# Kernel optimization log

Measured on AMD Instinct MI355X. Metric: run time of the kernel, lower is better.

The kernel has to match this reference:

```python
import jax, jax.numpy as jnp
import numpy as np
from jax import lax

N, CIN, COUT, KH, KW = 8, 32, 32, 3, 3
AUX, HID = 128, 256

def _prelu(z, a):
    return jnp.where(z >= 0, z, a * z)

def setup_inputs() -> dict:
    key = jax.random.key(0)
    ks = jax.random.split(key, 16)
    k = float(np.sqrt(1.0 / (CIN * KH * KW)))
    x = jax.random.normal(ks[0], (N, CIN, 384, 384), dtype=jnp.float32)
    y = jax.random.normal(ks[1], (N, AUX), dtype=jnp.float32)
    weight = jax.random.uniform(ks[2], (COUT, CIN, KH, KW), minval=-k, maxval=k, dtype=jnp.float32)
    mod_out = COUT * CIN * KH * KW
    s1 = float(np.sqrt(1.0 / AUX)); s2 = float(np.sqrt(1.0 / HID))
    fc_w1 = jax.random.uniform(ks[3], (AUX, HID), minval=-s1, maxval=s1, dtype=jnp.float32)
    fc_b1 = jax.random.uniform(ks[4], (HID,), minval=-s1, maxval=s1, dtype=jnp.float32)
    fc_a = jnp.asarray(0.25, dtype=jnp.float32)  # PReLU default init
    fc_w2 = jax.random.uniform(ks[5], (HID, mod_out), minval=-s2, maxval=s2, dtype=jnp.float32)
    fc_b2 = jax.random.uniform(ks[6], (mod_out,), minval=-s2, maxval=s2, dtype=jnp.float32)
    b_w1 = jax.random.uniform(ks[7], (AUX, HID), minval=-s1, maxval=s1, dtype=jnp.float32)
    b_b1 = jax.random.uniform(ks[8], (HID,), minval=-s1, maxval=s1, dtype=jnp.float32)
    b_a = jnp.asarray(0.25, dtype=jnp.float32)
    b_w2 = jax.random.uniform(ks[9], (HID, COUT), minval=-s2, maxval=s2, dtype=jnp.float32)
    b_b2 = jax.random.uniform(ks[10], (COUT,), minval=-s2, maxval=s2, dtype=jnp.float32)
    return {"x": x, "y": y, "weight": weight,
            "fc_w1": fc_w1, "fc_b1": fc_b1, "fc_a": fc_a, "fc_w2": fc_w2, "fc_b2": fc_b2,
            "b_w1": b_w1, "b_b1": b_b1, "b_a": b_a, "b_w2": b_w2, "b_b2": b_b2}

def reference(x, y, weight, fc_w1, fc_b1, fc_a, fc_w2, fc_b2, b_w1, b_b1, b_a, b_w2, b_b2):
    # Modulation MLP: Linear -> PReLU -> Linear -> Sigmoid
    h = _prelu(y @ fc_w1 + fc_b1, fc_a)
    mod = jax.nn.sigmoid(h @ fc_w2 + fc_b2)            # (N, COUT*CIN*KH*KW)
    w_mod = mod.reshape(N, COUT, CIN, KH, KW) * weight  # per-sample kernels

    # Per-sample conv2d, stride 1, padding 1 (SAME-like for k=3)
    def conv1(xi, wi):  # xi: (CIN,H,W), wi: (COUT,CIN,KH,KW)
        o = lax.conv_general_dilated(xi[None], wi, window_strides=(1, 1),
                                     padding=[(1, 1), (1, 1)],
                                     dimension_numbers=("NCHW", "OIHW", "NCHW"))
        return o[0]
    out = jax.vmap(conv1)(x, w_mod)                     # (N, COUT, H, W)

    # Learned bias MLP: Linear -> PReLU -> Linear
    hb = _prelu(y @ b_w1 + b_b1, b_a)
    bias = hb @ b_w2 + b_b2                             # (N, COUT)
    return out + bias[:, :, None, None]
```

## Files before the change

### kernel.cpp

```cpp
#include <hip/hip_runtime.h>
#include <math.h>

#define N_    8
#define CIN   32
#define COUT  32
#define AUX   128
#define HID   256
#define HWD   384
#define HW2   (HWD*HWD)
#define MODOUT (COUT*CIN*9)

typedef short s8v  __attribute__((ext_vector_type(8)));
typedef float f16v __attribute__((ext_vector_type(16)));

__device__ __forceinline__ unsigned short f2b(float f) {
    unsigned u = __float_as_uint(f);
    u += 0x7FFF + ((u >> 16) & 1);
    return (unsigned short)(u >> 16);
}
__device__ __forceinline__ float prelu_f(float z, float a) { return z >= 0.f ? z : a * z; }

__global__ __launch_bounds__(256) void mlp_head(
    const float* __restrict__ y,
    const float* __restrict__ fc_w1, const float* __restrict__ fc_b1, const float* __restrict__ fc_a,
    const float* __restrict__ b_w1,  const float* __restrict__ b_b1,  const float* __restrict__ b_a,
    const float* __restrict__ b_w2,  const float* __restrict__ b_b2,
    float* __restrict__ ws_h, float* __restrict__ ws_bias)
{
    __shared__ float ly[AUX];
    __shared__ float lhb[HID];
    const int n = blockIdx.x;
    const int j = threadIdx.x;
    if (j < AUX) ly[j] = y[n*AUX + j];
    __syncthreads();
    float ha = fc_b1[j];
    float hb = b_b1[j];
    for (int k = 0; k < AUX; ++k) {
        const float yv = ly[k];
        ha += yv * fc_w1[k*HID + j];
        hb += yv * b_w1[k*HID + j];
    }
    ws_h[n*HID + j] = prelu_f(ha, fc_a[0]);
    lhb[j] = prelu_f(hb, b_a[0]);
    __syncthreads();
    if (j < COUT) {
        float acc = b_b2[j];
        for (int k = 0; k < HID; ++k) acc += lhb[k] * b_w2[k*COUT + j];
        ws_bias[n*COUT + j] = acc;
    }
}

__global__ __launch_bounds__(256) void mod_weights(
    const float* __restrict__ ws_h,
    const float* __restrict__ fc_w2, const float* __restrict__ fc_b2,
    const float* __restrict__ weight, unsigned short* __restrict__ wmod)
{
    __shared__ float lh[N_*HID];
    __shared__ float red[8][32][N_];
    const int tid = threadIdx.x;
    for (int i = tid; i < N_*HID; i += 256) lh[i] = ws_h[i];
    __syncthreads();
    const int ml = tid & 31;
    const int jc = tid >> 5;
    const int m  = blockIdx.x * 32 + ml;
    float acc[N_];
#pragma unroll
    for (int n = 0; n < N_; ++n) acc[n] = 0.f;
    for (int jj = 0; jj < 32; ++jj) {
        const int j = jc*32 + jj;
        const float w = fc_w2[j*MODOUT + m];
#pragma unroll
        for (int n = 0; n < N_; ++n) acc[n] += lh[n*HID + j] * w;
    }
#pragma unroll
    for (int n = 0; n < N_; ++n) red[jc][ml][n] = acc[n];
    __syncthreads();
    const int nn = jc;
    float s = fc_b2[m];
#pragma unroll
    for (int k = 0; k < 8; ++k) s += red[k][ml][nn];
    const float mod = 1.f / (1.f + __expf(-s));
    const float v = mod * weight[m];
    const int co = m / 288, r = m - co*288;
    const int ci = r / 9,  tap = r - ci*9;
    wmod[((nn*9 + tap)*COUT + co)*CIN + ci] = f2b(v);
}

#define TH    8
#define TCOL  64
#define LROWS 10
#define LCOLS 72

__global__ __launch_bounds__(256, 2) void conv_mfma(
    const float* __restrict__ x,
    const unsigned short* __restrict__ wmod,
    const float* __restrict__ bias,
    float* __restrict__ out)
{
    __shared__ __align__(16) unsigned short lx[LROWS*LCOLS*16];

    const int tid = threadIdx.x;
    const int n   = blockIdx.z;
    const int gh  = blockIdx.y * TH;
    const int gw  = blockIdx.x * TCOL;
    const int lane = tid & 63;
    const int wv  = tid >> 6;
    const int lm  = lane & 31;
    const int h   = lane >> 5;

    f16v acc[4];
#pragma unroll
    for (int g = 0; g < 4; ++g)
#pragma unroll
        for (int r = 0; r < 16; ++r) acc[g][r] = 0.f;

    float br[16];
#pragma unroll
    for (int r = 0; r < 16; ++r) {
        const int co = (r & 3) + 8*(r >> 2) + 4*h;
        br[r] = bias[n*COUT + co];
    }

    for (int cc = 0; cc < 2; ++cc) {
        if (cc) __syncthreads();
        for (int it = tid; it < 360; it += 256) {
            const int o   = it & 1;
            const int rc  = it >> 1;
            const int row = rc / 18;
            const int q   = rc - row*18;
            const int gr  = gh + row - 1;
            const int gc  = gw + q*4 - 4;
            float va[8][4];
            if ((unsigned)gr < HWD && (unsigned)gc < HWD) {
                const float* xb = x + ((size_t)(n*CIN + cc*16 + o*8)*HWD + gr)*HWD + gc;
#pragma unroll
                for (int ci = 0; ci < 8; ++ci) {
                    const float4 t = *(const float4*)(xb + (size_t)ci*HW2);
                    va[ci][0] = t.x; va[ci][1] = t.y; va[ci][2] = t.z; va[ci][3] = t.w;
                }
            } else {
#pragma unroll
                for (int ci = 0; ci < 8; ++ci)
                    va[ci][0] = va[ci][1] = va[ci][2] = va[ci][3] = 0.f;
            }
#pragma unroll
            for (int c = 0; c < 4; ++c) {
                const unsigned w0 = (unsigned)f2b(va[0][c]) | ((unsigned)f2b(va[1][c]) << 16);
                const unsigned w1 = (unsigned)f2b(va[2][c]) | ((unsigned)f2b(va[3][c]) << 16);
                const unsigned w2 = (unsigned)f2b(va[4][c]) | ((unsigned)f2b(va[5][c]) << 16);
                const unsigned w3 = (unsigned)f2b(va[6][c]) | ((unsigned)f2b(va[7][c]) << 16);
                const int idx = ((row*LCOLS + q*4 + c)*16) + o*8;
                *(int4*)&lx[idx] = make_int4((int)w0, (int)w1, (int)w2, (int)w3);
            }
        }
        __syncthreads();

        s8v a[9];
#pragma unroll
        for (int t = 0; t < 9; ++t)
            a[t] = *(const s8v*)&wmod[(((n*9 + t)*COUT + lm)*CIN) + cc*16 + h*8];

#pragma unroll
        for (int g = 0; g < 4; ++g) {
            const int rr   = 2*wv + (g & 1);
            const int cg   = g >> 1;
            const int colb = cg*32 + lm + 3;
#pragma unroll
            for (int kh = 0; kh < 3; ++kh) {
                const int rowb = (rr + kh) * LCOLS;
#pragma unroll
                for (int kw = 0; kw < 3; ++kw) {
                    const s8v b = *(const s8v*)&lx[(rowb + colb + kw)*16 + h*8];
                    acc[g] = __builtin_amdgcn_mfma_f32_32x32x16_bf16(a[kh*3 + kw], b, acc[g], 0, 0, 0);
                }
            }
        }
    }

#pragma unroll
    for (int g = 0; g < 4; ++g) {
        const int rr = 2*wv + (g & 1);
        const int cg = g >> 1;
        float* ob = out + (size_t)(n*COUT)*HW2 + (size_t)(gh + rr)*HWD + gw + cg*32 + lm;
#pragma unroll
        for (int r = 0; r < 16; ++r) {
            const int co = (r & 3) + 8*(r >> 2) + 4*h;
            ob[(size_t)co*HW2] = acc[g][r] + br[r];
        }
    }
}

extern "C" void kernel_launch(void* const* d_in, const int* in_sizes, int n_in,
                              void* d_out, int out_size, void* d_ws, size_t ws_size,
                              hipStream_t stream) {
    const float* x     = (const float*)d_in[0];
    const float* y     = (const float*)d_in[1];
    const float* weight= (const float*)d_in[2];
    const float* fc_w1 = (const float*)d_in[3];
    const float* fc_b1 = (const float*)d_in[4];
    const float* fc_a  = (const float*)d_in[5];
    const float* fc_w2 = (const float*)d_in[6];
    const float* fc_b2 = (const float*)d_in[7];
    const float* b_w1  = (const float*)d_in[8];
    const float* b_b1  = (const float*)d_in[9];
    const float* b_a   = (const float*)d_in[10];
    const float* b_w2  = (const float*)d_in[11];
    const float* b_b2  = (const float*)d_in[12];
    float* out = (float*)d_out;

    unsigned short* ws_wmod = (unsigned short*)d_ws;
    float* ws_h    = (float*)((char*)d_ws + (size_t)MODOUT*N_*2);
    float* ws_bias = ws_h + N_*HID;

    mlp_head<<<N_, 256, 0, stream>>>(y, fc_w1, fc_b1, fc_a, b_w1, b_b1, b_a,
                                     b_w2, b_b2, ws_h, ws_bias);
    mod_weights<<<MODOUT/32, 256, 0, stream>>>(ws_h, fc_w2, fc_b2, weight, ws_wmod);
    conv_mfma<<<dim3(HWD/TCOL, HWD/TH, N_), 256, 0, stream>>>(x, ws_wmod, ws_bias, out);
}
```

Before: 329.5 us.

## Fuse MLP kernels and stage all input channels at once in conv

The two small MLP kernels are merged into one. Every block now recomputes the first hidden layer for all samples, which removes a launch and a workspace round trip. The conv kernel stages all 32 input channels in shared memory in a single pass, using a padded channel stride to reduce bank conflicts, and drops one barrier. It loads both weight halves into registers up front and accumulates one output group at a time, so fewer accumulator registers are live and occupancy can rise to 3 blocks. The cost is more LDS per block and redundant first-layer work across the 288 MLP blocks.

```diff
diff --git a/kernel.cpp b/kernel.cpp
--- a/kernel.cpp
+++ b/kernel.cpp
@@ -11,6 +11,7 @@
 #define MODOUT (COUT*CIN*9)
 
 typedef short s8v  __attribute__((ext_vector_type(8)));
+typedef short s4v  __attribute__((ext_vector_type(4)));
 typedef float f16v __attribute__((ext_vector_type(16)));
 
 __device__ __forceinline__ unsigned short f2b(float f) {
@@ -20,84 +21,94 @@
 }
 __device__ __forceinline__ float prelu_f(float z, float a) { return z >= 0.f ? z : a * z; }
 
-__global__ __launch_bounds__(256) void mlp_head(
+__global__ __launch_bounds__(256) void mod_all(
     const float* __restrict__ y,
     const float* __restrict__ fc_w1, const float* __restrict__ fc_b1, const float* __restrict__ fc_a,
+    const float* __restrict__ fc_w2, const float* __restrict__ fc_b2,
+    const float* __restrict__ weight,
     const float* __restrict__ b_w1,  const float* __restrict__ b_b1,  const float* __restrict__ b_a,
     const float* __restrict__ b_w2,  const float* __restrict__ b_b2,
-    float* __restrict__ ws_h, float* __restrict__ ws_bias)
+    unsigned short* __restrict__ wmod, float* __restrict__ ws_bias)
 {
-    __shared__ float ly[AUX];
-    __shared__ float lhb[HID];
-    const int n = blockIdx.x;
-    const int j = threadIdx.x;
-    if (j < AUX) ly[j] = y[n*AUX + j];
-    __syncthreads();
-    float ha = fc_b1[j];
-    float hb = b_b1[j];
-    for (int k = 0; k < AUX; ++k) {
-        const float yv = ly[k];
-        ha += yv * fc_w1[k*HID + j];
-        hb += yv * b_w1[k*HID + j];
-    }
-    ws_h[n*HID + j] = prelu_f(ha, fc_a[0]);
-    lhb[j] = prelu_f(hb, b_a[0]);
-    __syncthreads();
-    if (j < COUT) {
-        float acc = b_b2[j];
-        for (int k = 0; k < HID; ++k) acc += lhb[k] * b_w2[k*COUT + j];
-        ws_bias[n*COUT + j] = acc;
-    }
-}
-
-__global__ __launch_bounds__(256) void mod_weights(
-    const float* __restrict__ ws_h,
-    const float* __restrict__ fc_w2, const float* __restrict__ fc_b2,
-    const float* __restrict__ weight, unsigned short* __restrict__ wmod)
-{
+    __shared__ float ly[N_*AUX];
     __shared__ float lh[N_*HID];
     __shared__ float red[8][32][N_];
     const int tid = threadIdx.x;
-    for (int i = tid; i < N_*HID; i += 256) lh[i] = ws_h[i];
-    __syncthreads();
-    const int ml = tid & 31;
-    const int jc = tid >> 5;
+    for (int i = tid; i < N_*AUX; i += 256) ly[i] = y[i];
+    __syncthreads();
+    {
+        const int j = tid;
+        const float b1 = fc_b1[j];
+        float hacc[N_];
+#pragma unroll
+        for (int n = 0; n < N_; ++n) hacc[n] = b1;
+        for (int k = 0; k < AUX; ++k) {
+            const float w = fc_w1[k*HID + j];
+#pragma unroll
+            for (int n = 0; n < N_; ++n) hacc[n] += ly[n*AUX + k] * w;
+        }
+        const float a1 = fc_a[0];
+#pragma unroll
+        for (int n = 0; n < N_; ++n) lh[n*HID + j] = prelu_f(hacc[n], a1);
+    }
+    __syncthreads();
+    const int ml = tid & 31, jc = tid >> 5;
     const int m  = blockIdx.x * 32 + ml;
-    float acc[N_];
-#pragma unroll
-    for (int n = 0; n < N_; ++n) acc[n] = 0.f;
-    for (int jj = 0; jj < 32; ++jj) {
-        const int j = jc*32 + jj;
-        const float w = fc_w2[j*MODOUT + m];
-#pragma unroll
-        for (int n = 0; n < N_; ++n) acc[n] += lh[n*HID + j] * w;
-    }
-#pragma unroll
-    for (int n = 0; n < N_; ++n) red[jc][ml][n] = acc[n];
-    __syncthreads();
-    const int nn = jc;
-    float s = fc_b2[m];
-#pragma unroll
-    for (int k = 0; k < 8; ++k) s += red[k][ml][nn];
-    const float mod = 1.f / (1.f + __expf(-s));
-    const float v = mod * weight[m];
-    const int co = m / 288, r = m - co*288;
-    const int ci = r / 9,  tap = r - ci*9;
-    wmod[((nn*9 + tap)*COUT + co)*CIN + ci] = f2b(v);
-}
-
-#define TH    8
-#define TCOL  64
-#define LROWS 10
-#define LCOLS 72
-
-__global__ __launch_bounds__(256, 2) void conv_mfma(
+    {
+        float acc[N_];
+#pragma unroll
+        for (int n = 0; n < N_; ++n) acc[n] = 0.f;
+        for (int jj = 0; jj < 32; ++jj) {
+            const int j = jc*32 + jj;
+            const float w = fc_w2[j*MODOUT + m];
+#pragma unroll
+            for (int n = 0; n < N_; ++n) acc[n] += lh[n*HID + j] * w;
+        }
+#pragma unroll
+        for (int n = 0; n < N_; ++n) red[jc][ml][n] = acc[n];
+    }
+    __syncthreads();
+    {
+        const int nn = jc;
+        float s = fc_b2[m];
+#pragma unroll
+        for (int k = 0; k < 8; ++k) s += red[k][ml][nn];
+        const float mod = 1.f / (1.f + __expf(-s));
+        const float v = mod * weight[m];
+        const int co = m / 288, r = m - co*288;
+        const int ci = r / 9,  tap = r - ci*9;
+        wmod[((nn*9 + tap)*COUT + co)*CIN + ci] = f2b(v);
+    }
+    if (blockIdx.x < N_) {
+        const int n = blockIdx.x;
+        const int j = tid;
+        float hb = b_b1[j];
+        for (int k = 0; k < AUX; ++k) hb += ly[n*AUX + k] * b_w1[k*HID + j];
+        __syncthreads();
+        float* sc = &red[0][0][0];
+        sc[j] = prelu_f(hb, b_a[0]);
+        __syncthreads();
+        if (j < COUT) {
+            float s = b_b2[j];
+            for (int k = 0; k < HID; ++k) s += sc[k] * b_w2[k*COUT + j];
+            ws_bias[n*COUT + j] = s;
+        }
+    }
+}
+
+#define TH   8
+#define TCOL 64
+#define CS   36
+#define LC   72
+#define RS   (LC*CS)
+
+__global__ __launch_bounds__(256, 3) void conv_mfma(
     const float* __restrict__ x,
     const unsigned short* __restrict__ wmod,
     const float* __restrict__ bias,
     float* __restrict__ out)
 {
-    __shared__ __align__(16) unsigned short lx[LROWS*LCOLS*16];
+    __shared__ short lx[10*RS];
 
     const int tid = threadIdx.x;
     const int n   = blockIdx.z;
@@ -108,11 +119,12 @@
     const int lm  = lane & 31;
     const int h   = lane >> 5;
 
-    f16v acc[4];
-#pragma unroll
-    for (int g = 0; g < 4; ++g)
-#pragma unroll
-        for (int r = 0; r < 16; ++r) acc[g][r] = 0.f;
+    s8v a[2][9];
+#pragma unroll
+    for (int cc = 0; cc < 2; ++cc)
+#pragma unroll
+        for (int t = 0; t < 9; ++t)
+            a[cc][t] = *(const s8v*)&wmod[(((n*9 + t)*COUT + lm)*CIN) + cc*16 + h*8];
 
     float br[16];
 #pragma unroll
@@ -121,71 +133,67 @@
         br[r] = bias[n*COUT + co];
     }
 
-    for (int cc = 0; cc < 2; ++cc) {
-        if (cc) __syncthreads();
-        for (int it = tid; it < 360; it += 256) {
-            const int o   = it & 1;
-            const int rc  = it >> 1;
-            const int row = rc / 18;
-            const int q   = rc - row*18;
-            const int gr  = gh + row - 1;
-            const int gc  = gw + q*4 - 4;
-            float va[8][4];
-            if ((unsigned)gr < HWD && (unsigned)gc < HWD) {
-                const float* xb = x + ((size_t)(n*CIN + cc*16 + o*8)*HWD + gr)*HWD + gc;
-#pragma unroll
-                for (int ci = 0; ci < 8; ++ci) {
-                    const float4 t = *(const float4*)(xb + (size_t)ci*HW2);
-                    va[ci][0] = t.x; va[ci][1] = t.y; va[ci][2] = t.z; va[ci][3] = t.w;
-                }
-            } else {
-#pragma unroll
-                for (int ci = 0; ci < 8; ++ci)
-                    va[ci][0] = va[ci][1] = va[ci][2] = va[ci][3] = 0.f;
+    for (int it = tid; it < 720; it += 256) {
+        const int o   = it & 3;
+        const int rc  = it >> 2;
+        const int row = rc / 18;
+        const int q   = rc - row*18;
+        const int gr  = gh + row - 1;
+        const int gc  = gw + q*4 - 4;
+        float va[8][4];
+        if ((unsigned)gr < HWD && (unsigned)gc < HWD) {
+            const float* xb = x + ((size_t)(n*CIN + o*8)*HWD + gr)*HWD + gc;
+#pragma unroll
+            for (int ci = 0; ci < 8; ++ci) {
+                const float4 t = *(const float4*)(xb + (size_t)ci*HW2);
+                va[ci][0] = t.x; va[ci][1] = t.y; va[ci][2] = t.z; va[ci][3] = t.w;
             }
-#pragma unroll
-            for (int c = 0; c < 4; ++c) {
-                const unsigned w0 = (unsigned)f2b(va[0][c]) | ((unsigned)f2b(va[1][c]) << 16);
-                const unsigned w1 = (unsigned)f2b(va[2][c]) | ((unsigned)f2b(va[3][c]) << 16);
-                const unsigned w2 = (unsigned)f2b(va[4][c]) | ((unsigned)f2b(va[5][c]) << 16);
-                const unsigned w3 = (unsigned)f2b(va[6][c]) | ((unsigned)f2b(va[7][c]) << 16);
-                const int idx = ((row*LCOLS + q*4 + c)*16) + o*8;
-                *(int4*)&lx[idx] = make_int4((int)w0, (int)w1, (int)w2, (int)w3);
-            }
-        }
-        __syncthreads();
-
-        s8v a[9];
-#pragma unroll
-        for (int t = 0; t < 9; ++t)
-            a[t] = *(const s8v*)&wmod[(((n*9 + t)*COUT + lm)*CIN) + cc*16 + h*8];
-
-#pragma unroll
-        for (int g = 0; g < 4; ++g) {
-            const int rr   = 2*wv + (g & 1);
-            const int cg   = g >> 1;
-            const int colb = cg*32 + lm + 3;
-#pragma unroll
-            for (int kh = 0; kh < 3; ++kh) {
-                const int rowb = (rr + kh) * LCOLS;
-#pragma unroll
-                for (int kw = 0; kw < 3; ++kw) {
-                    const s8v b = *(const s8v*)&lx[(rowb + colb + kw)*16 + h*8];
-                    acc[g] = __builtin_amdgcn_mfma_f32_32x32x16_bf16(a[kh*3 + kw], b, acc[g], 0, 0, 0);
-                }
-            }
-        }
-    }
+        } else {
+#pragma unroll
+            for (int ci = 0; ci < 8; ++ci)
+                va[ci][0] = va[ci][1] = va[ci][2] = va[ci][3] = 0.f;
+        }
+#pragma unroll
+        for (int c = 0; c < 4; ++c) {
+            const unsigned w0 = (unsigned)f2b(va[0][c]) | ((unsigned)f2b(va[1][c]) << 16);
+            const unsigned w1 = (unsigned)f2b(va[2][c]) | ((unsigned)f2b(va[3][c]) << 16);
+            const unsigned w2 = (unsigned)f2b(va[4][c]) | ((unsigned)f2b(va[5][c]) << 16);
+            const unsigned w3 = (unsigned)f2b(va[6][c]) | ((unsigned)f2b(va[7][c]) << 16);
+            const int idx = row*RS + (q*4 + c)*CS + o*8;
+            *(int2*)&lx[idx]     = make_int2((int)w0, (int)w1);
+            *(int2*)&lx[idx + 4] = make_int2((int)w2, (int)w3);
+        }
+    }
+    __syncthreads();
 
 #pragma unroll
     for (int g = 0; g < 4; ++g) {
         const int rr = 2*wv + (g & 1);
         const int cg = g >> 1;
+        f16v acc;
+#pragma unroll
+        for (int r = 0; r < 16; ++r) acc[r] = 0.f;
+#pragma unroll
+        for (int cc = 0; cc < 2; ++cc) {
+            const int q8 = (cc*2 + h) * 8;
+#pragma unroll
+            for (int kh = 0; kh < 3; ++kh) {
+                const int rowb = (rr + kh)*RS + q8;
+#pragma unroll
+                for (int kw = 0; kw < 3; ++kw) {
+                    const int off = rowb + (cg*32 + lm + 3 + kw)*CS;
+                    union { s8v v; s4v hf[2]; } ub;
+                    ub.hf[0] = *(const s4v*)&lx[off];
+                    ub.hf[1] = *(const s4v*)&lx[off + 4];
+                    acc = __builtin_amdgcn_mfma_f32_32x32x16_bf16(a[cc][kh*3 + kw], ub.v, acc, 0, 0, 0);
+                }
+            }
+        }
         float* ob = out + (size_t)(n*COUT)*HW2 + (size_t)(gh + rr)*HWD + gw + cg*32 + lm;
 #pragma unroll
         for (int r = 0; r < 16; ++r) {
             const int co = (r & 3) + 8*(r >> 2) + 4*h;
-            ob[(size_t)co*HW2] = acc[g][r] + br[r];
+            ob[(size_t)co*HW2] = acc[r] + br[r];
         }
     }
 }
@@ -209,11 +217,10 @@
     float* out = (float*)d_out;
 
     unsigned short* ws_wmod = (unsigned short*)d_ws;
-    float* ws_h    = (float*)((char*)d_ws + (size_t)MODOUT*N_*2);
-    float* ws_bias = ws_h + N_*HID;
-
-    mlp_head<<<N_, 256, 0, stream>>>(y, fc_w1, fc_b1, fc_a, b_w1, b_b1, b_a,
-                                     b_w2, b_b2, ws_h, ws_bias);
-    mod_weights<<<MODOUT/32, 256, 0, stream>>>(ws_h, fc_w2, fc_b2, weight, ws_wmod);
+    float* ws_bias = (float*)((char*)d_ws + (size_t)MODOUT*N_*2);
+
+    mod_all<<<MODOUT/32, 256, 0, stream>>>(y, fc_w1, fc_b1, fc_a, fc_w2, fc_b2,
+                                           weight, b_w1, b_b1, b_a, b_w2, b_b2,
+                                           ws_wmod, ws_bias);
     conv_mfma<<<dim3(HWD/TCOL, HWD/TH, N_), 256, 0, stream>>>(x, ws_wmod, ws_bias, out);
 }
```

Result: slower. 386.9 us (+17.4%).
